# Optimization experiments

Measured on AMD Instinct MI355X. Metric: run time of the kernel, lower is better.

Reference implementation:

```python
import jax, jax.numpy as jnp
import numpy as np

IN_DIM = 768   # 256 + 256 + 128 + 128
OUT_DIM = 256
N_EDGES = 320000
N_GRAPHS = 64


def setup_inputs() -> dict:
    key = jax.random.key(0)
    ks = jax.random.split(key, 7)
    src = jax.random.normal(ks[0], (N_EDGES, 256), dtype=jnp.float32)
    dest = jax.random.normal(ks[1], (N_EDGES, 256), dtype=jnp.float32)
    edge_attr = jax.random.normal(ks[2], (N_EDGES, 128), dtype=jnp.float32)
    u = jax.random.normal(ks[3], (N_GRAPHS, 128), dtype=jnp.float32)
    batch = jnp.sort(jax.random.randint(ks[4], (N_EDGES,), 0, N_GRAPHS, dtype=jnp.int64)) if jax.config.read('jax_enable_x64') else jnp.sort(jax.random.randint(ks[4], (N_EDGES,), 0, N_GRAPHS)).astype(jnp.int32)
    # Linear(in_dim, out_dim): torch default init ~ U(-1/sqrt(in), 1/sqrt(in))
    bound = 1.0 / np.sqrt(IN_DIM)
    W = jax.random.uniform(ks[5], (IN_DIM, OUT_DIM), dtype=jnp.float32, minval=-bound, maxval=bound)
    b = jax.random.uniform(ks[6], (OUT_DIM,), dtype=jnp.float32, minval=-bound, maxval=bound)
    return {"src": src, "dest": dest, "edge_attr": edge_attr, "u": u, "batch": batch, "W": W, "b": b}


def reference(src, dest, edge_attr, u, batch, W, b):
    # u_expanded = u[batch]; concat [dest, src, edge_attr, u_exp]; Linear + ReLU
    u_exp = jnp.take(u, batch, axis=0)                    # [E, 128]
    combined = jnp.concatenate([dest, src, edge_attr, u_exp], axis=1)  # [E, 768]
    out = combined @ W + b                                # [E, 256]
    return jax.nn.relu(out)
```

## Files before the change

### kernel.cpp

```cpp
#include <hip/hip_runtime.h>
#include <cstdint>
#include <cstddef>

#define BM 128
#define BN 256
#define BK 64
#define KT_STEPS 12
#define THREADS 512
#define LDS_A_BYTES (BM * BK * 2)
#define LDS_B_BYTES (BN * BK * 2)
#define LDS_BUF_BYTES (LDS_A_BYTES + LDS_B_BYTES)
#define LDS_TOTAL (2 * LDS_BUF_BYTES)

typedef __attribute__((ext_vector_type(4))) float f32x4;
typedef __attribute__((ext_vector_type(8))) short bf16x8;

__device__ __forceinline__ unsigned short f2bf(float f) {
  union { float f; uint32_t u; } v; v.f = f;
  uint32_t r = v.u + 0x7FFFu + ((v.u >> 16) & 1u);
  return (unsigned short)(r >> 16);
}

__device__ __forceinline__ bf16x8 cvt8(f32x4 a, f32x4 b) {
  bf16x8 r;
  r[0] = (short)f2bf(a[0]); r[1] = (short)f2bf(a[1]);
  r[2] = (short)f2bf(a[2]); r[3] = (short)f2bf(a[3]);
  r[4] = (short)f2bf(b[0]); r[5] = (short)f2bf(b[1]);
  r[6] = (short)f2bf(b[2]); r[7] = (short)f2bf(b[3]);
  return r;
}

__global__ void wt_kernel(const float* __restrict__ W, unsigned short* __restrict__ WtS) {
  const int c8 = blockIdx.x;
  const int n  = threadIdx.x;
  float v[8];
#pragma unroll
  for (int i = 0; i < 8; ++i) v[i] = W[(size_t)(c8 * 8 + i) * 256 + n];
  f32x4 a = {v[0], v[1], v[2], v[3]};
  f32x4 b = {v[4], v[5], v[6], v[7]};
  size_t off = (size_t)n * 1536 + (size_t)(c8 >> 3) * 128
             + (((c8 & 7) * 16) ^ ((n & 7) << 4));
  *(bf16x8*)((char*)WtS + off) = cvt8(a, b);
}

__global__ __launch_bounds__(THREADS, 2) void edge_gemm(
    const float* __restrict__ srcf, const float* __restrict__ destf,
    const float* __restrict__ eaf, const float* __restrict__ uf,
    const int* __restrict__ batch, const unsigned short* __restrict__ WtS,
    const float* __restrict__ bias, float* __restrict__ out)
{
  extern __shared__ char smem[];
  const int tid  = threadIdx.x;
  const int lane = tid & 63;
  const int w    = tid >> 6;
  const int wr   = w >> 2;
  const int wc   = w & 3;
  const int m0   = blockIdx.x * BM;
  const int l15  = lane & 15;
  const int l4   = lane >> 4;

  const int ar = tid >> 2;
  const int aq = tid & 3;
  const int ae = m0 + ar;

  float bs[4];
#pragma unroll
  for (int nf = 0; nf < 4; ++nf) bs[nf] = bias[wc * 64 + nf * 16 + l15];

  f32x4 acc[4][4];
  f32x4 z = {0.f, 0.f, 0.f, 0.f};
#pragma unroll
  for (int i = 0; i < 4; ++i)
#pragma unroll
    for (int j = 0; j < 4; ++j) acc[i][j] = z;

  auto a_ptr = [&](int kt) -> const float* {
    const int coff = aq * 16;
    if (kt < 4)  return destf + (size_t)ae * 256 + kt * 64 + coff;
    if (kt < 8)  return srcf  + (size_t)ae * 256 + (kt - 4) * 64 + coff;
    if (kt < 10) return eaf   + (size_t)ae * 128 + (kt - 8) * 64 + coff;
    return uf + (size_t)batch[ae] * 128 + (kt - 10) * 64 + coff;
  };

  f32x4 va0, va1, va2, va3;
  auto load_a = [&](int kt) {
    const float* p = a_ptr(kt);
    va0 = *(const f32x4*)(p);
    va1 = *(const f32x4*)(p + 4);
    va2 = *(const f32x4*)(p + 8);
    va3 = *(const f32x4*)(p + 12);
  };
  auto write_a = [&](int buf) {
    char* Ab = smem + buf * LDS_BUF_BYTES;
    const int base = ar * 128;
    const int sw = (ar & 7) << 4;
    *(bf16x8*)(Ab + base + ((aq * 32)      ^ sw)) = cvt8(va0, va1);
    *(bf16x8*)(Ab + base + ((aq * 32 + 16) ^ sw)) = cvt8(va2, va3);
  };
  auto stage_b = [&](int buf, int kt) {
    char* Bb = smem + buf * LDS_BUF_BYTES + LDS_A_BYTES;
    const char* wb = (const char*)WtS + kt * 128;
#pragma unroll
    for (int j = 0; j < 4; ++j) {
      const int chunk = j * 512 + tid;
      const int n = chunk >> 3, c = chunk & 7;
      const char* g = wb + (size_t)n * 1536 + c * 16;
      char* l = Bb + (size_t)(j * 512 + w * 64) * 16;
      __builtin_amdgcn_global_load_lds(
          (const __attribute__((address_space(1))) uint32_t*)g,
          (__attribute__((address_space(3))) uint32_t*)l, 16, 0, 0);
    }
  };
  auto compute = [&](int buf) {
    const char* Ab = smem + buf * LDS_BUF_BYTES;
    const char* Bb = Ab + LDS_A_BYTES;
#pragma unroll
    for (int ks = 0; ks < 2; ++ks) {
      const int kbyte = ks * 64 + l4 * 16;
      bf16x8 af[4], bfr[4];
#pragma unroll
      for (int mf = 0; mf < 4; ++mf) {
        const int r = wr * 64 + mf * 16 + l15;
        af[mf] = *(const bf16x8*)(Ab + r * 128 + (kbyte ^ ((r & 7) << 4)));
      }
#pragma unroll
      for (int nf = 0; nf < 4; ++nf) {
        const int cn = wc * 64 + nf * 16 + l15;
        bfr[nf] = *(const bf16x8*)(Bb + cn * 128 + (kbyte ^ ((cn & 7) << 4)));
      }
#pragma unroll
      for (int mf = 0; mf < 4; ++mf)
#pragma unroll
        for (int nf = 0; nf < 4; ++nf)
          acc[mf][nf] = __builtin_amdgcn_mfma_f32_16x16x32_bf16(
              af[mf], bfr[nf], acc[mf][nf], 0, 0, 0);
    }
  };

  load_a(0);
  stage_b(0, 0);
  write_a(0);
  __syncthreads();

  int cur = 0;
  for (int kt = 0; kt < KT_STEPS; ++kt) {
    const bool more = (kt + 1 < KT_STEPS);
    if (more) {
      load_a(kt + 1);
      stage_b(cur ^ 1, kt + 1);
    }
    compute(cur);
    if (more) write_a(cur ^ 1);
    __syncthreads();
    cur ^= 1;
  }

#pragma unroll
  for (int mf = 0; mf < 4; ++mf) {
    const int r0 = m0 + wr * 64 + mf * 16 + l4 * 4;
#pragma unroll
    for (int nf = 0; nf < 4; ++nf) {
      const int cn = wc * 64 + nf * 16 + l15;
      const f32x4 v = acc[mf][nf];
#pragma unroll
      for (int j = 0; j < 4; ++j) {
        const float x = v[j] + bs[nf];
        out[(size_t)(r0 + j) * 256 + cn] = x > 0.f ? x : 0.f;
      }
    }
  }
}

extern "C" void kernel_launch(void* const* d_in, const int* in_sizes, int n_in,
                              void* d_out, int out_size, void* d_ws, size_t ws_size,
                              hipStream_t stream) {
  const float* srcf  = (const float*)d_in[0];
  const float* destf = (const float*)d_in[1];
  const float* eaf   = (const float*)d_in[2];
  const float* uf    = (const float*)d_in[3];
  const int*   batch = (const int*)d_in[4];
  const float* W     = (const float*)d_in[5];
  const float* bias  = (const float*)d_in[6];
  float* out = (float*)d_out;
  unsigned short* WtS = (unsigned short*)d_ws;

  wt_kernel<<<96, 256, 0, stream>>>(W, WtS);

  hipFuncSetAttribute((const void*)edge_gemm,
                      hipFuncAttributeMaxDynamicSharedMemorySize, LDS_TOTAL);
  edge_gemm<<<320000 / BM, THREADS, LDS_TOTAL, stream>>>(
      srcf, destf, eaf, uf, batch, WtS, bias, out);
}
```

Measured before the change: 312.3 us.

## Halve K tile, use fragment-major LDS layout, target four blocks per CU

Shrinks the K step from 64 to 32 (24 steps), which halves LDS per block and the A prefetch registers, and raises launch bounds to 4 blocks per CU. The weight pre-pass now writes B in a fragment-major tiled layout so each MFMA fragment is read from LDS contiguously without an XOR swizzle. The A tile uses the same fragment-major layout. The aim is more resident waves to hide global-load latency. In exchange there are twice as many barriers per tile, and the tighter register cap under launch bounds 4 may cause spills.

```diff
diff --git a/kernel.cpp b/kernel.cpp
--- a/kernel.cpp
+++ b/kernel.cpp
@@ -4,8 +4,8 @@
 
 #define BM 128
 #define BN 256
-#define BK 64
-#define KT_STEPS 12
+#define BK 32
+#define KT_STEPS 24
 #define THREADS 512
 #define LDS_A_BYTES (BM * BK * 2)
 #define LDS_B_BYTES (BN * BK * 2)
@@ -31,19 +31,20 @@
 }
 
 __global__ void wt_kernel(const float* __restrict__ W, unsigned short* __restrict__ WtS) {
-  const int c8 = blockIdx.x;
-  const int n  = threadIdx.x;
+  const int gid = blockIdx.x * 256 + threadIdx.x;
+  const int kt = gid >> 10;
+  const int c  = gid & 1023;
+  const int n  = ((c >> 6) << 4) | (c & 15);
+  const int k0 = kt * 32 + ((c >> 4) & 3) * 8;
   float v[8];
 #pragma unroll
-  for (int i = 0; i < 8; ++i) v[i] = W[(size_t)(c8 * 8 + i) * 256 + n];
+  for (int i = 0; i < 8; ++i) v[i] = W[(size_t)(k0 + i) * 256 + n];
   f32x4 a = {v[0], v[1], v[2], v[3]};
   f32x4 b = {v[4], v[5], v[6], v[7]};
-  size_t off = (size_t)n * 1536 + (size_t)(c8 >> 3) * 128
-             + (((c8 & 7) * 16) ^ ((n & 7) << 4));
-  *(bf16x8*)((char*)WtS + off) = cvt8(a, b);
+  *(bf16x8*)((char*)WtS + (size_t)gid * 16) = cvt8(a, b);
 }
 
-__global__ __launch_bounds__(THREADS, 2) void edge_gemm(
+__global__ __launch_bounds__(THREADS, 4) void edge_gemm(
     const float* __restrict__ srcf, const float* __restrict__ destf,
     const float* __restrict__ eaf, const float* __restrict__ uf,
     const int* __restrict__ batch, const unsigned short* __restrict__ WtS,
@@ -75,36 +76,29 @@
     for (int j = 0; j < 4; ++j) acc[i][j] = z;
 
   auto a_ptr = [&](int kt) -> const float* {
-    const int coff = aq * 16;
-    if (kt < 4)  return destf + (size_t)ae * 256 + kt * 64 + coff;
-    if (kt < 8)  return srcf  + (size_t)ae * 256 + (kt - 4) * 64 + coff;
-    if (kt < 10) return eaf   + (size_t)ae * 128 + (kt - 8) * 64 + coff;
-    return uf + (size_t)batch[ae] * 128 + (kt - 10) * 64 + coff;
+    const int coff = aq * 8;
+    if (kt < 8)  return destf + (size_t)ae * 256 + kt * 32 + coff;
+    if (kt < 16) return srcf  + (size_t)ae * 256 + (kt - 8) * 32 + coff;
+    if (kt < 20) return eaf   + (size_t)ae * 128 + (kt - 16) * 32 + coff;
+    return uf + (size_t)batch[ae] * 128 + (kt - 20) * 32 + coff;
   };
 
-  f32x4 va0, va1, va2, va3;
+  f32x4 va0, va1;
   auto load_a = [&](int kt) {
     const float* p = a_ptr(kt);
     va0 = *(const f32x4*)(p);
     va1 = *(const f32x4*)(p + 4);
-    va2 = *(const f32x4*)(p + 8);
-    va3 = *(const f32x4*)(p + 12);
   };
   auto write_a = [&](int buf) {
     char* Ab = smem + buf * LDS_BUF_BYTES;
-    const int base = ar * 128;
-    const int sw = (ar & 7) << 4;
-    *(bf16x8*)(Ab + base + ((aq * 32)      ^ sw)) = cvt8(va0, va1);
-    *(bf16x8*)(Ab + base + ((aq * 32 + 16) ^ sw)) = cvt8(va2, va3);
+    *(bf16x8*)(Ab + (ar >> 4) * 1024 + aq * 256 + (ar & 15) * 16) = cvt8(va0, va1);
   };
   auto stage_b = [&](int buf, int kt) {
     char* Bb = smem + buf * LDS_BUF_BYTES + LDS_A_BYTES;
-    const char* wb = (const char*)WtS + kt * 128;
+    const char* wb = (const char*)WtS + (size_t)kt * 16384;
 #pragma unroll
-    for (int j = 0; j < 4; ++j) {
-      const int chunk = j * 512 + tid;
-      const int n = chunk >> 3, c = chunk & 7;
-      const char* g = wb + (size_t)n * 1536 + c * 16;
+    for (int j = 0; j < 2; ++j) {
+      const char* g = wb + (size_t)(j * 512 + tid) * 16;
       char* l = Bb + (size_t)(j * 512 + w * 64) * 16;
       __builtin_amdgcn_global_load_lds(
           (const __attribute__((address_space(1))) uint32_t*)g,
@@ -114,27 +108,19 @@
   auto compute = [&](int buf) {
     const char* Ab = smem + buf * LDS_BUF_BYTES;
     const char* Bb = Ab + LDS_A_BYTES;
+    bf16x8 af[4], bfr[4];
 #pragma unroll
-    for (int ks = 0; ks < 2; ++ks) {
-      const int kbyte = ks * 64 + l4 * 16;
-      bf16x8 af[4], bfr[4];
+    for (int mf = 0; mf < 4; ++mf)
+      af[mf] = *(const bf16x8*)(Ab + (wr * 4 + mf) * 1024 + l4 * 256 + l15 * 16);
 #pragma unroll
-      for (int mf = 0; mf < 4; ++mf) {
-        const int r = wr * 64 + mf * 16 + l15;
-        af[mf] = *(const bf16x8*)(Ab + r * 128 + (kbyte ^ ((r & 7) << 4)));
-      }
+    for (int nf = 0; nf < 4; ++nf)
+      bfr[nf] = *(const bf16x8*)(Bb + (wc * 4 + nf) * 1024 + l4 * 256 + l15 * 16);
 #pragma unroll
-      for (int nf = 0; nf < 4; ++nf) {
-        const int cn = wc * 64 + nf * 16 + l15;
-        bfr[nf] = *(const bf16x8*)(Bb + cn * 128 + (kbyte ^ ((cn & 7) << 4)));
-      }
+    for (int mf = 0; mf < 4; ++mf)
 #pragma unroll
-      for (int mf = 0; mf < 4; ++mf)
-#pragma unroll
-        for (int nf = 0; nf < 4; ++nf)
-          acc[mf][nf] = __builtin_amdgcn_mfma_f32_16x16x32_bf16(
-              af[mf], bfr[nf], acc[mf][nf], 0, 0, 0);
-    }
+      for (int nf = 0; nf < 4; ++nf)
+        acc[mf][nf] = __builtin_amdgcn_mfma_f32_16x16x32_bf16(
+            af[mf], bfr[nf], acc[mf][nf], 0, 0, 0);
   };
 
   load_a(0);
```

Measured after the change: 258.2 us. 1.21x faster.
